# Optimization experiments

Measured on AMD Instinct MI355X. Metric: run time of the kernel, lower is better.

## Reference

```python
import jax, jax.numpy as jnp
import numpy as np

HEAD_SIZE = 64
D_MODEL = 1024


def setup_inputs() -> dict:
    key = jax.random.key(0)
    ks = jax.random.split(key, 6)
    B, S, D, H = 4, 4096, D_MODEL, HEAD_SIZE
    q = jax.random.normal(ks[0], (B, S, D), dtype=jnp.float32)
    k = jax.random.normal(ks[1], (B, S, D), dtype=jnp.float32)
    v = jax.random.normal(ks[2], (B, S, D), dtype=jnp.float32)
    # Linear(d_model, head_size, bias=False): stored as [D, H] so x @ W
    scale = 1.0 / np.sqrt(D)
    w_q = jax.random.normal(ks[3], (D, H), dtype=jnp.float32) * scale
    w_k = jax.random.normal(ks[4], (D, H), dtype=jnp.float32) * scale
    w_v = jax.random.normal(ks[5], (D, H), dtype=jnp.float32) * scale
    return {"q": q, "k": k, "v": v, "w_q": w_q, "w_k": w_k, "w_v": w_v}


def reference(q, k, v, w_q, w_k, w_v):
    # project: [B,S,D] @ [D,H] -> [B,S,H]
    qh = q @ w_q
    kh = k @ w_k
    vh = v @ w_v
    H = qh.shape[-1]
    # scores [B,S,S], scaled by head_size**-0.5
    rel = jnp.einsum('bqh,bkh->bqk', qh, kh) * (H ** -0.5)
    S = rel.shape[-1]
    causal = jnp.tril(jnp.ones((S, S), dtype=bool))
    rel = jnp.where(causal, rel, -jnp.inf)
    weights = jax.nn.softmax(rel, axis=-1)
    return jnp.einsum('bqk,bkh->bqh', weights, vh)
```

## Files before the change

kernel.cpp:

```cpp
#include <hip/hip_runtime.h>
#include <hip/hip_bf16.h>
#include <cstdint>

#define D_MODEL 1024
#define HEAD    64
#define SEQ     4096
#define BATCH   4
#define NROWS   (BATCH * SEQ)

typedef __attribute__((ext_vector_type(8))) short short8;
typedef __attribute__((ext_vector_type(4))) float floatx4;

__device__ __forceinline__ ushort f2bf(float f) {
    union { __hip_bfloat16 h; ushort u; } c;
    c.h = __float2bfloat16(f);
    return c.u;
}
__device__ __forceinline__ uint pk2(float a, float b) {
    return (uint)f2bf(a) | ((uint)f2bf(b) << 16);
}

__device__ __forceinline__ void gload16(const void* g, void* l) {
    __builtin_amdgcn_global_load_lds(
        (const __attribute__((address_space(1))) unsigned int*)g,
        (__attribute__((address_space(3))) unsigned int*)l, 16, 0, 0);
}

__global__ __launch_bounds__(256) void wprep_kernel(
    const float* __restrict__ wq, const float* __restrict__ wk,
    const float* __restrict__ wv, ushort* __restrict__ wt)
{
    const int which = blockIdx.y;
    const int k0    = blockIdx.x * 64;
    const float* w  = (which == 0) ? wq : (which == 1) ? wk : wv;
    const int tid   = threadIdx.x;

    __shared__ ushort lds[64][65];

#pragma unroll
    for (int i = 0; i < 16; ++i) {
        int idx = tid + 256 * i;
        int kl  = idx >> 6;
        int n   = idx & 63;
        lds[n][kl] = f2bf(w[(size_t)(k0 + kl) * 64 + n]);
    }
    __syncthreads();
#pragma unroll
    for (int i = 0; i < 16; ++i) {
        int idx = tid + 256 * i;
        int n   = idx >> 6;
        int kl  = idx & 63;
        wt[(size_t)(which * 64 + n) * D_MODEL + k0 + kl] = lds[n][kl];
    }
}

__global__ __launch_bounds__(256) void proj_kernel(
    const float* __restrict__ xq, const float* __restrict__ xk,
    const float* __restrict__ xv, const ushort* __restrict__ wt,
    ushort* __restrict__ qh, ushort* __restrict__ kh, ushort* __restrict__ vt)
{
    const int which = blockIdx.y;
    const float*  x = (which == 0) ? xq : (which == 1) ? xk : xv;
    const ushort* w = wt + (size_t)which * 64 * D_MODEL;

    const int row0 = blockIdx.x * 64;
    const int tid  = threadIdx.x;
    const int wv   = tid >> 6;
    const int ln   = tid & 63;
    const int l16  = ln & 15;
    const int quad = ln >> 4;

    __shared__ float  Abuf[2][64 * 64];
    __shared__ ushort Wbuf[2][64 * 64];

    const float* asrc[4];
#pragma unroll
    for (int i = 0; i < 4; ++i) {
        int j  = wv * 4 + i;
        int lr = 4 * j + (ln >> 4);
        int cf = ((ln & 15) ^ (lr & 15)) * 4;
        asrc[i] = x + (size_t)(row0 + lr) * D_MODEL + cf;
    }
    const ushort* wsrc[2];
#pragma unroll
    for (int i = 0; i < 2; ++i) {
        int j  = wv * 2 + i;
        int n  = 8 * j + (ln >> 3);
        int kc = ((ln & 7) ^ (ln >> 3)) * 8;
        wsrc[i] = w + (size_t)n * D_MODEL + kc;
    }

    floatx4 acc[4] = {};

#define STAGE(buf, kk)                                                        \
    do {                                                                      \
        char* ab_ = (char*)&Abuf[buf][0];                                     \
        char* wb_ = (char*)&Wbuf[buf][0];                                     \
        _Pragma("unroll")                                                     \
        for (int i_ = 0; i_ < 4; ++i_)                                        \
            gload16(asrc[i_] + (kk), ab_ + (wv * 4 + i_) * 1024);             \
        _Pragma("unroll")                                                     \
        for (int i_ = 0; i_ < 2; ++i_)                                        \
            gload16(wsrc[i_] + (kk), wb_ + (wv * 2 + i_) * 1024);             \
    } while (0)

#define COMPUTE(buf)                                                          \
    do {                                                                      \
        const char* ab_ = (const char*)&Abuf[buf][0];                         \
        const char* wb_ = (const char*)&Wbuf[buf][0];                         \
        const int arow_ = wv * 16 + l16;                                      \
        const int akey_ = l16 << 4;                         \
        _Pragma("unroll")                                                     \
        for (int ks_ = 0; ks_ < 2; ++ks_) {                                   \
            const int colb_ = (ks_ * 32 + quad * 8) * 4;                      \
            float4 f0 = *(const float4*)(ab_ + arow_ * 256 + ((colb_)      ^ akey_)); \
            float4 f1 = *(const float4*)(ab_ + arow_ * 256 + ((colb_ + 16) ^ akey_)); \
            union { short8 s; uint u[4]; } a_;                                \
            a_.u[0] = pk2(f0.x, f0.y); a_.u[1] = pk2(f0.z, f0.w);             \
            a_.u[2] = pk2(f1.x, f1.y); a_.u[3] = pk2(f1.z, f1.w);             \
            const int wcolb_ = (ks_ * 32 + quad * 8) * 2;                     \
            const int wkey_  = (l16 & 7) << 4;     \
            _Pragma("unroll")                                                 \
            for (int nt_ = 0; nt_ < 4; ++nt_) {                               \
                const int n_ = nt_ * 16 + l16;                                \
                short8 bf_ = *(const short8*)(wb_ + n_ * 128 + (wcolb_ ^ wkey_)); \
                acc[nt_] = __builtin_amdgcn_mfma_f32_16x16x32_bf16(a_.s, bf_, acc[nt_], 0, 0, 0); \
            }                                                                 \
        }                                                                     \
    } while (0)

    STAGE(0, 0);
    STAGE(1, 64);
    for (int t = 0; t < 16; ++t) {
        if (t == 15) {
            asm volatile("s_waitcnt vmcnt(0)" ::: "memory");
        } else {
            asm volatile("s_waitcnt vmcnt(6)" ::: "memory");
        }
        __builtin_amdgcn_sched_barrier(0);
        __builtin_amdgcn_s_barrier();
        __builtin_amdgcn_sched_barrier(0);
        __builtin_amdgcn_s_setprio(1);
        COMPUTE(t & 1);
        __builtin_amdgcn_s_setprio(0);
        __builtin_amdgcn_sched_barrier(0);
        __builtin_amdgcn_s_barrier();
        __builtin_amdgcn_sched_barrier(0);
        if (t + 2 < 16) STAGE(t & 1, (t + 2) * 64);
    }
#undef STAGE
#undef COMPUTE

    const int rbase = row0 + wv * 16 + quad * 4;
    if (which < 2) {
        ushort* y = (which == 0) ? qh : kh;
        const float sc = (which == 0) ? 0.125f : 1.0f;
#pragma unroll
        for (int nt = 0; nt < 4; ++nt) {
            int h = nt * 16 + l16;
#pragma unroll
            for (int r = 0; r < 4; ++r)
                y[(size_t)(rbase + r) * HEAD + h] = f2bf(acc[nt][r] * sc);
        }
    } else {
        const int b  = rbase >> 12;
        const int s0 = rbase & (SEQ - 1);
#pragma unroll
        for (int nt = 0; nt < 4; ++nt) {
            int h = nt * 16 + l16;
            uint2 pk = make_uint2(pk2(acc[nt][0], acc[nt][1]), pk2(acc[nt][2], acc[nt][3]));
            *(uint2*)&vt[(size_t)(b * 64 + h) * SEQ + s0] = pk;
        }
    }
}

__global__ __launch_bounds__(256, 2) void attn_kernel(
    const ushort* __restrict__ qh, const ushort* __restrict__ kh,
    const ushort* __restrict__ vt, float* __restrict__ out)
{
    const int b    = blockIdx.x >> 7;
    const int i    = blockIdx.x & 127;
    const int qsA  = i, qsB = 255 - i;
    const int q0A  = qsA * 16, q0B = qsB * 16;
    const int nA   = (qsA >> 2) + 1;
    const int nB   = (qsB >> 2) + 1;
    const int tid  = threadIdx.x;
    const int wv   = tid >> 6;
    const int ln   = tid & 63;
    const int l16  = ln & 15;
    const int quad = ln >> 4;

    __shared__ ushort PA[4][16 * 72];
    __shared__ ushort PB[4][16 * 72];
    __shared__ float  Obuf[4][16][68];
    __shared__ float  Lbuf[4][16];

    const ushort* khb = kh + (size_t)b * SEQ * HEAD;
    const ushort* vtb = vt + (size_t)b * HEAD * SEQ;

    const size_t qbA = ((size_t)b * SEQ + q0A + l16) * HEAD + quad * 8;
    const size_t qbB = ((size_t)b * SEQ + q0B + l16) * HEAD + quad * 8;
    const short8 qA0 = *(const short8*)(qh + qbA);
    const short8 qA1 = *(const short8*)(qh + qbA + 32);
    const short8 qB0 = *(const short8*)(qh + qbB);
    const short8 qB1 = *(const short8*)(qh + qbB + 32);

    floatx4 OA[4] = {}, OB[4] = {};
    float rsA = 0.f, rsB = 0.f;
    ushort* myPA = PA[wv];
    ushort* myPB = PB[wv];

    const int cA = (nA > wv) ? (((nA - 1 - wv) >> 2) + 1) : 0;
    const int cB = ((nB - 1 - wv) >> 2) + 1;
    const int steps = (cA > cB) ? cA : cB;

    for (int s = 0; s < steps; ++s) {
        const int ktA = wv + 4 * s, ktB = wv + 4 * s;
        const bool doA = s < cA, doB = s < cB;
        const int k0A = ktA * 64, k0B = ktB * 64;

        short8 kfA[8], vfA[8], kfB[8], vfB[8];
        if (doA) {
#pragma unroll
            for (int nt = 0; nt < 4; ++nt) {
                const ushort* vp = vtb + (size_t)(nt * 16 + l16) * SEQ + k0A + quad * 8;
                vfA[nt * 2] = *(const short8*)vp; vfA[nt * 2 + 1] = *(const short8*)(vp + 32);
                const ushort* kp = khb + (size_t)(k0A + nt * 16 + l16) * HEAD + quad * 8;
                kfA[nt * 2] = *(const short8*)kp; kfA[nt * 2 + 1] = *(const short8*)(kp + 32);
            }
        }
        if (doB) {
#pragma unroll
            for (int nt = 0; nt < 4; ++nt) {
                const ushort* vp = vtb + (size_t)(nt * 16 + l16) * SEQ + k0B + quad * 8;
                vfB[nt * 2] = *(const short8*)vp; vfB[nt * 2 + 1] = *(const short8*)(vp + 32);
                const ushort* kp = khb + (size_t)(k0B + nt * 16 + l16) * HEAD + quad * 8;
                kfB[nt * 2] = *(const short8*)kp; kfB[nt * 2 + 1] = *(const short8*)(kp + 32);
            }
        }

        floatx4 aA[4], aB[4];
        if (doA) {
#pragma unroll
            for (int nt = 0; nt < 4; ++nt) {
                floatx4 c = {};
                c = __builtin_amdgcn_mfma_f32_16x16x32_bf16(kfA[nt * 2],     qA0, c, 0, 0, 0);
                c = __builtin_amdgcn_mfma_f32_16x16x32_bf16(kfA[nt * 2 + 1], qA1, c, 0, 0, 0);
                aA[nt] = c;
            }
        }
        if (doB) {
#pragma unroll
            for (int nt = 0; nt < 4; ++nt) {
                floatx4 c = {};
                c = __builtin_amdgcn_mfma_f32_16x16x32_bf16(kfB[nt * 2],     qB0, c, 0, 0, 0);
                c = __builtin_amdgcn_mfma_f32_16x16x32_bf16(kfB[nt * 2 + 1], qB1, c, 0, 0, 0);
                aB[nt] = c;
            }
        }

        if (doA) {
            const bool masked = (ktA == nA - 1);
#pragma unroll
            for (int nt = 0; nt < 4; ++nt) {
                union { ushort u[4]; uint2 w; } pk;
#pragma unroll
                for (int r = 0; r < 4; ++r) {
                    float sv = aA[nt][r];
                    if (masked && (k0A + nt * 16 + quad * 4 + r > q0A + l16)) sv = -3.0e38f;
                    float p = __expf(sv);
                    rsA += p;
                    pk.u[r] = f2bf(p);
                }
                *(uint2*)&myPA[l16 * 72 + nt * 16 + quad * 4] = pk.w;
            }
        }
        if (doB) {
            const bool masked = (ktB == nB - 1);
#pragma unroll
            for (int nt = 0; nt < 4; ++nt) {
                union { ushort u[4]; uint2 w; } pk;
#pragma unroll
                for (int r = 0; r < 4; ++r) {
                    float sv = aB[nt][r];
                    if (masked && (k0B + nt * 16 + quad * 4 + r > q0B + l16)) sv = -3.0e38f;
                    float p = __expf(sv);
                    rsB += p;
                    pk.u[r] = f2bf(p);
                }
                *(uint2*)&myPB[l16 * 72 + nt * 16 + quad * 4] = pk.w;
            }
        }

        if (doA) {
            short8 p0 = *(const short8*)&myPA[l16 * 72 + quad * 8];
            short8 p1 = *(const short8*)&myPA[l16 * 72 + 32 + quad * 8];
#pragma unroll
            for (int nt = 0; nt < 4; ++nt) {
                OA[nt] = __builtin_amdgcn_mfma_f32_16x16x32_bf16(p0, vfA[nt * 2],     OA[nt], 0, 0, 0);
                OA[nt] = __builtin_amdgcn_mfma_f32_16x16x32_bf16(p1, vfA[nt * 2 + 1], OA[nt], 0, 0, 0);
            }
        }
        if (doB) {
            short8 p0 = *(const short8*)&myPB[l16 * 72 + quad * 8];
            short8 p1 = *(const short8*)&myPB[l16 * 72 + 32 + quad * 8];
#pragma unroll
            for (int nt = 0; nt < 4; ++nt) {
                OB[nt] = __builtin_amdgcn_mfma_f32_16x16x32_bf16(p0, vfB[nt * 2],     OB[nt], 0, 0, 0);
                OB[nt] = __builtin_amdgcn_mfma_f32_16x16x32_bf16(p1, vfB[nt * 2 + 1], OB[nt], 0, 0, 0);
            }
        }
    }

    rsA += __shfl_xor(rsA, 16); rsA += __shfl_xor(rsA, 32);
    if (quad == 0) Lbuf[wv][l16] = rsA;
#pragma unroll
    for (int nt = 0; nt < 4; ++nt)
#pragma unroll
        for (int r = 0; r < 4; ++r)
            Obuf[wv][quad * 4 + r][nt * 16 + l16] = OA[nt][r];
    __syncthreads();
    {
        const int row = tid >> 4, h0 = (tid & 15) * 4;
        float l = Lbuf[0][row] + Lbuf[1][row] + Lbuf[2][row] + Lbuf[3][row];
        float inv = 1.f / l;
        float4 o;
        o.x = (Obuf[0][row][h0+0] + Obuf[1][row][h0+0] + Obuf[2][row][h0+0] + Obuf[3][row][h0+0]) * inv;
        o.y = (Obuf[0][row][h0+1] + Obuf[1][row][h0+1] + Obuf[2][row][h0+1] + Obuf[3][row][h0+1]) * inv;
        o.z = (Obuf[0][row][h0+2] + Obuf[1][row][h0+2] + Obuf[2][row][h0+2] + Obuf[3][row][h0+2]) * inv;
        o.w = (Obuf[0][row][h0+3] + Obuf[1][row][h0+3] + Obuf[2][row][h0+3] + Obuf[3][row][h0+3]) * inv;
        *(float4*)&out[((size_t)b * SEQ + q0A + row) * HEAD + h0] = o;
    }
    __syncthreads();

    rsB += __shfl_xor(rsB, 16); rsB += __shfl_xor(rsB, 32);
    if (quad == 0) Lbuf[wv][l16] = rsB;
#pragma unroll
    for (int nt = 0; nt < 4; ++nt)
#pragma unroll
        for (int r = 0; r < 4; ++r)
            Obuf[wv][quad * 4 + r][nt * 16 + l16] = OB[nt][r];
    __syncthreads();
    {
        const int row = tid >> 4, h0 = (tid & 15) * 4;
        float l = Lbuf[0][row] + Lbuf[1][row] + Lbuf[2][row] + Lbuf[3][row];
        float inv = 1.f / l;
        float4 o;
        o.x = (Obuf[0][row][h0+0] + Obuf[1][row][h0+0] + Obuf[2][row][h0+0] + Obuf[3][row][h0+0]) * inv;
        o.y = (Obuf[0][row][h0+1] + Obuf[1][row][h0+1] + Obuf[2][row][h0+1] + Obuf[3][row][h0+1]) * inv;
        o.z = (Obuf[0][row][h0+2] + Obuf[1][row][h0+2] + Obuf[2][row][h0+2] + Obuf[3][row][h0+2]) * inv;
        o.w = (Obuf[0][row][h0+3] + Obuf[1][row][h0+3] + Obuf[2][row][h0+3] + Obuf[3][row][h0+3]) * inv;
        *(float4*)&out[((size_t)b * SEQ + q0B + row) * HEAD + h0] = o;
    }
}

extern "C" void kernel_launch(void* const* d_in, const int* in_sizes, int n_in,
                              void* d_out, int out_size, void* d_ws, size_t ws_size,
                              hipStream_t stream) {
    const float* q  = (const float*)d_in[0];
    const float* k  = (const float*)d_in[1];
    const float* v  = (const float*)d_in[2];
    const float* wq = (const float*)d_in[3];
    const float* wk = (const float*)d_in[4];
    const float* wv = (const float*)d_in[5];

    ushort* qh = (ushort*)d_ws;
    ushort* kh = qh + (size_t)NROWS * HEAD;
    ushort* vt = kh + (size_t)NROWS * HEAD;
    ushort* wt = vt + (size_t)NROWS * HEAD;

    dim3 wgrid(D_MODEL / 64, 3);
    wprep_kernel<<<wgrid, 256, 0, stream>>>(wq, wk, wv, wt);

    dim3 pgrid(NROWS / 64, 3);
    proj_kernel<<<pgrid, 256, 0, stream>>>(q, k, v, wt, qh, kh, vt);

    attn_kernel<<<BATCH * 128, 256, 0, stream>>>(qh, kh, vt, (float*)d_out);
}
```

Before: 273.1 us.

## Split attention key tiles across six waves and raise MFMA priority

The attention block grows from four waves to six (384 threads), and the causal key tiles are distributed round-robin across six waves instead of four. The shared A/B tile index is unified, and the partial-sum reduction now loops over six wave buffers. s_setprio is raised around the MFMA sections to favour matrix issue. More waves per block add latency hiding and shorten the per-wave serial chain. In exchange, shared memory grows and occupancy per CU may drop under the new launch bounds.

```diff
diff --git a/kernel.cpp b/kernel.cpp
--- a/kernel.cpp
+++ b/kernel.cpp
@@ -174,7 +174,7 @@
     }
 }
 
-__global__ __launch_bounds__(256, 2) void attn_kernel(
+__global__ __launch_bounds__(384, 3) void attn_kernel(
     const ushort* __restrict__ qh, const ushort* __restrict__ kh,
     const ushort* __restrict__ vt, float* __restrict__ out)
 {
@@ -190,10 +190,10 @@
     const int l16  = ln & 15;
     const int quad = ln >> 4;
 
-    __shared__ ushort PA[4][16 * 72];
-    __shared__ ushort PB[4][16 * 72];
-    __shared__ float  Obuf[4][16][68];
-    __shared__ float  Lbuf[4][16];
+    __shared__ ushort PA[6][16 * 72];
+    __shared__ ushort PB[6][16 * 72];
+    __shared__ float  Obuf[6][16][68];
+    __shared__ float  Lbuf[6][16];
 
     const ushort* khb = kh + (size_t)b * SEQ * HEAD;
     const ushort* vtb = vt + (size_t)b * HEAD * SEQ;
@@ -210,36 +210,37 @@
     ushort* myPA = PA[wv];
     ushort* myPB = PB[wv];
 
-    const int cA = (nA > wv) ? (((nA - 1 - wv) >> 2) + 1) : 0;
-    const int cB = ((nB - 1 - wv) >> 2) + 1;
+    const int cA = (nA > wv) ? (((nA - 1 - wv) / 6) + 1) : 0;
+    const int cB = (nB > wv) ? (((nB - 1 - wv) / 6) + 1) : 0;
     const int steps = (cA > cB) ? cA : cB;
 
     for (int s = 0; s < steps; ++s) {
-        const int ktA = wv + 4 * s, ktB = wv + 4 * s;
+        const int kt = wv + 6 * s;
         const bool doA = s < cA, doB = s < cB;
-        const int k0A = ktA * 64, k0B = ktB * 64;
+        const int k0 = kt * 64;
 
         short8 kfA[8], vfA[8], kfB[8], vfB[8];
         if (doA) {
 #pragma unroll
             for (int nt = 0; nt < 4; ++nt) {
-                const ushort* vp = vtb + (size_t)(nt * 16 + l16) * SEQ + k0A + quad * 8;
+                const ushort* vp = vtb + (size_t)(nt * 16 + l16) * SEQ + k0 + quad * 8;
                 vfA[nt * 2] = *(const short8*)vp; vfA[nt * 2 + 1] = *(const short8*)(vp + 32);
-                const ushort* kp = khb + (size_t)(k0A + nt * 16 + l16) * HEAD + quad * 8;
+                const ushort* kp = khb + (size_t)(k0 + nt * 16 + l16) * HEAD + quad * 8;
                 kfA[nt * 2] = *(const short8*)kp; kfA[nt * 2 + 1] = *(const short8*)(kp + 32);
             }
         }
         if (doB) {
 #pragma unroll
             for (int nt = 0; nt < 4; ++nt) {
-                const ushort* vp = vtb + (size_t)(nt * 16 + l16) * SEQ + k0B + quad * 8;
+                const ushort* vp = vtb + (size_t)(nt * 16 + l16) * SEQ + k0 + quad * 8;
                 vfB[nt * 2] = *(const short8*)vp; vfB[nt * 2 + 1] = *(const short8*)(vp + 32);
-                const ushort* kp = khb + (size_t)(k0B + nt * 16 + l16) * HEAD + quad * 8;
+                const ushort* kp = khb + (size_t)(k0 + nt * 16 + l16) * HEAD + quad * 8;
                 kfB[nt * 2] = *(const short8*)kp; kfB[nt * 2 + 1] = *(const short8*)(kp + 32);
             }
         }
 
         floatx4 aA[4], aB[4];
+        __builtin_amdgcn_s_setprio(1);
         if (doA) {
 #pragma unroll
             for (int nt = 0; nt < 4; ++nt) {
@@ -258,16 +259,17 @@
                 aB[nt] = c;
             }
         }
+        __builtin_amdgcn_s_setprio(0);
 
         if (doA) {
-            const bool masked = (ktA == nA - 1);
+            const bool masked = (kt == nA - 1);
 #pragma unroll
             for (int nt = 0; nt < 4; ++nt) {
                 union { ushort u[4]; uint2 w; } pk;
 #pragma unroll
                 for (int r = 0; r < 4; ++r) {
                     float sv = aA[nt][r];
-                    if (masked && (k0A + nt * 16 + quad * 4 + r > q0A + l16)) sv = -3.0e38f;
+                    if (masked && (k0 + nt * 16 + quad * 4 + r > q0A + l16)) sv = -3.0e38f;
                     float p = __expf(sv);
                     rsA += p;
                     pk.u[r] = f2bf(p);
@@ -276,14 +278,14 @@
             }
         }
         if (doB) {
-            const bool masked = (ktB == nB - 1);
+            const bool masked = (kt == nB - 1);
 #pragma unroll
             for (int nt = 0; nt < 4; ++nt) {
                 union { ushort u[4]; uint2 w; } pk;
 #pragma unroll
                 for (int r = 0; r < 4; ++r) {
                     float sv = aB[nt][r];
-                    if (masked && (k0B + nt * 16 + quad * 4 + r > q0B + l16)) sv = -3.0e38f;
+                    if (masked && (k0 + nt * 16 + quad * 4 + r > q0B + l16)) sv = -3.0e38f;
                     float p = __expf(sv);
                     rsB += p;
                     pk.u[r] = f2bf(p);
@@ -292,6 +294,7 @@
             }
         }
 
+        __builtin_amdgcn_s_setprio(1);
         if (doA) {
             short8 p0 = *(const short8*)&myPA[l16 * 72 + quad * 8];
             short8 p1 = *(const short8*)&myPA[l16 * 72 + 32 + quad * 8];
@@ -310,6 +313,7 @@
                 OB[nt] = __builtin_amdgcn_mfma_f32_16x16x32_bf16(p1, vfB[nt * 2 + 1], OB[nt], 0, 0, 0);
             }
         }
+        __builtin_amdgcn_s_setprio(0);
     }
 
     rsA += __shfl_xor(rsA, 16); rsA += __shfl_xor(rsA, 32);
@@ -320,15 +324,21 @@
         for (int r = 0; r < 4; ++r)
             Obuf[wv][quad * 4 + r][nt * 16 + l16] = OA[nt][r];
     __syncthreads();
-    {
+    if (tid < 256) {
         const int row = tid >> 4, h0 = (tid & 15) * 4;
-        float l = Lbuf[0][row] + Lbuf[1][row] + Lbuf[2][row] + Lbuf[3][row];
+        float l = 0.f;
+#pragma unroll
+        for (int wq_ = 0; wq_ < 6; ++wq_) l += Lbuf[wq_][row];
         float inv = 1.f / l;
-        float4 o;
-        o.x = (Obuf[0][row][h0+0] + Obuf[1][row][h0+0] + Obuf[2][row][h0+0] + Obuf[3][row][h0+0]) * inv;
-        o.y = (Obuf[0][row][h0+1] + Obuf[1][row][h0+1] + Obuf[2][row][h0+1] + Obuf[3][row][h0+1]) * inv;
-        o.z = (Obuf[0][row][h0+2] + Obuf[1][row][h0+2] + Obuf[2][row][h0+2] + Obuf[3][row][h0+2]) * inv;
-        o.w = (Obuf[0][row][h0+3] + Obuf[1][row][h0+3] + Obuf[2][row][h0+3] + Obuf[3][row][h0+3]) * inv;
+        float4 o = make_float4(0.f, 0.f, 0.f, 0.f);
+#pragma unroll
+        for (int wq_ = 0; wq_ < 6; ++wq_) {
+            o.x += Obuf[wq_][row][h0 + 0];
+            o.y += Obuf[wq_][row][h0 + 1];
+            o.z += Obuf[wq_][row][h0 + 2];
+            o.w += Obuf[wq_][row][h0 + 3];
+        }
+        o.x *= inv; o.y *= inv; o.z *= inv; o.w *= inv;
         *(float4*)&out[((size_t)b * SEQ + q0A + row) * HEAD + h0] = o;
     }
     __syncthreads();
@@ -341,15 +351,21 @@
         for (int r = 0; r < 4; ++r)
             Obuf[wv][quad * 4 + r][nt * 16 + l16] = OB[nt][r];
     __syncthreads();
-    {
+    if (tid < 256) {
         const int row = tid >> 4, h0 = (tid & 15) * 4;
-        float l = Lbuf[0][row] + Lbuf[1][row] + Lbuf[2][row] + Lbuf[3][row];
+        float l = 0.f;
+#pragma unroll
+        for (int wq_ = 0; wq_ < 6; ++wq_) l += Lbuf[wq_][row];
         float inv = 1.f / l;
-        float4 o;
-        o.x = (Obuf[0][row][h0+0] + Obuf[1][row][h0+0] + Obuf[2][row][h0+0] + Obuf[3][row][h0+0]) * inv;
-        o.y = (Obuf[0][row][h0+1] + Obuf[1][row][h0+1] + Obuf[2][row][h0+1] + Obuf[3][row][h0+1]) * inv;
-        o.z = (Obuf[0][row][h0+2] + Obuf[1][row][h0+2] + Obuf[2][row][h0+2] + Obuf[3][row][h0+2]) * inv;
-        o.w = (Obuf[0][row][h0+3] + Obuf[1][row][h0+3] + Obuf[2][row][h0+3] + Obuf[3][row][h0+3]) * inv;
+        float4 o = make_float4(0.f, 0.f, 0.f, 0.f);
+#pragma unroll
+        for (int wq_ = 0; wq_ < 6; ++wq_) {
+            o.x += Obuf[wq_][row][h0 + 0];
+            o.y += Obuf[wq_][row][h0 + 1];
+            o.z += Obuf[wq_][row][h0 + 2];
+            o.w += Obuf[wq_][row][h0 + 3];
+        }
+        o.x *= inv; o.y *= inv; o.z *= inv; o.w *= inv;
         *(float4*)&out[((size_t)b * SEQ + q0B + row) * HEAD + h0] = o;
     }
 }
@@ -375,5 +391,5 @@
     dim3 pgrid(NROWS / 64, 3);
     proj_kernel<<<pgrid, 256, 0, stream>>>(q, k, v, wt, qh, kh, vt);
 
-    attn_kernel<<<BATCH * 128, 256, 0, stream>>>(qh, kh, vt, (float*)d_out);
-}
+    attn_kernel<<<BATCH * 128, 384, 0, stream>>>(qh, kh, vt, (float*)d_out);
+}
```

After: 407.7 us. +49.3%, slower.
